# Kernel optimization log

Hardware: AMD Instinct MI355X
Metric: run time of the kernel (lower is better)

## Reference

```python
import jax, jax.numpy as jnp
import numpy as np

N_NODES = 50000
N_EDGES = 800000
IN, HID, OUT = 128, 128, 64


def _mean_agg(h, src, dst, n):
    # gather source-node features along edges, segment-mean into destination nodes
    msgs = h[src]                                          # [E, d]
    summ = jax.ops.segment_sum(msgs, dst, num_segments=n)  # [N, d]
    deg = jax.ops.segment_sum(jnp.ones((src.shape[0],), h.dtype), dst, num_segments=n)
    return summ / jnp.maximum(deg, 1.0)[:, None]           # zero-in-degree -> 0


def _sage_layer(h, src, dst, W_self, W_neigh, b, n):
    # DGL SAGEConv mean: fc_self(h) + fc_neigh(mean_neigh(h)) + bias
    agg = _mean_agg(h, src, dst, n)
    return h @ W_self + agg @ W_neigh + b


def setup_inputs() -> dict:
    key = jax.random.key(0)
    ks = jax.random.split(key, 8)
    s = 1.0 / np.sqrt(IN)
    return {
        "feat": jax.random.normal(ks[0], (N_NODES, IN), jnp.float32),
        "src": jax.random.randint(ks[1], (N_EDGES,), 0, N_NODES, jnp.int64),
        "dst": jax.random.randint(ks[2], (N_EDGES,), 0, N_NODES, jnp.int64),
        "W_self1": jax.random.normal(ks[3], (IN, HID), jnp.float32) * s,
        "W_neigh1": jax.random.normal(ks[4], (IN, HID), jnp.float32) * s,
        "b1": jnp.zeros((HID,), jnp.float32),
        "W_self2": jax.random.normal(ks[5], (HID, OUT), jnp.float32) * (1.0 / np.sqrt(HID)),
        "W_neigh2": jax.random.normal(ks[6], (HID, OUT), jnp.float32) * (1.0 / np.sqrt(HID)),
        "b2": jnp.zeros((OUT,), jnp.float32),
    }


def reference(feat, src, dst, W_self1, W_neigh1, b1, W_self2, W_neigh2, b2):
    n = feat.shape[0]
    h = _sage_layer(feat, src, dst, W_self1, W_neigh1, b1, n)
    h = jax.nn.relu(h)  # dropout is identity in eval mode
    h = _sage_layer(h, src, dst, W_self2, W_neigh2, b2, n)
    return h
```

## Files before the change

### kernel.cpp

```cpp
#include <hip/hip_runtime.h>

#define N_NODES 50000
#define N_EDGES 800000

typedef unsigned short ushort_t;
typedef unsigned int uint_t;
typedef __attribute__((ext_vector_type(8))) short bf16x8;
typedef __attribute__((ext_vector_type(4))) float f32x4;

#define NB 196
#define BCAP 6144
#define SDEPTH 16
#define EPB 1024
#define NBLK_BUCKET ((N_EDGES + EPB - 1) / EPB)

#define IOFF_ROWPTR  100000
#define IOFF_EIDX    150016
#define IOFF_BBASE   950016
#define IOFF_BCNT    950528
#define UOFF_WT      1920000
#define UOFF_FEATB   2000000
#define UOFF_AGG1B   8400000
#define UOFF_H1B     14800000
#define UOFF_P2B     21200000

__device__ __forceinline__ float bf2f(uint_t u) {
    return __uint_as_float(u << 16);
}
__device__ __forceinline__ uint_t f2bf(float f) {
    uint_t x = __float_as_uint(f);
    return (x + 0x7FFFu + ((x >> 16) & 1u)) >> 16;
}

__global__ __launch_bounds__(256) void bucket_kernel(const int* __restrict__ src,
                                                     const int* __restrict__ dst,
                                                     uint_t* __restrict__ bucket,
                                                     int* __restrict__ bcnt) {
    __shared__ uint_t stage[NB][SDEPTH];
    __shared__ int lcnt[NB];
    __shared__ int gbase[NB];
    int tid = threadIdx.x;
    for (int i = tid; i < NB; i += 256) lcnt[i] = 0;
    __syncthreads();
    int e0 = blockIdx.x * EPB;
#pragma unroll
    for (int it = 0; it < EPB / 256; ++it) {
        int e = e0 + it * 256 + tid;
        if (e < N_EDGES) {
            int d = dst[e], s = src[e];
            uint_t v = ((uint_t)d << 16) | (uint_t)s;
            int b = d >> 8;
            int slot = atomicAdd(&lcnt[b], 1);
            if (slot < SDEPTH) {
                stage[b][slot] = v;
            } else {
                int p = atomicAdd(&bcnt[b], 1);
                bucket[(long)b * BCAP + p] = v;
            }
        }
    }
    __syncthreads();
    if (tid < NB) {
        int n = min(lcnt[tid], SDEPTH);
        gbase[tid] = (n > 0) ? atomicAdd(&bcnt[tid], n) : 0;
    }
    __syncthreads();
    for (int s = tid; s < NB * SDEPTH; s += 256) {
        int b = s >> 4, i = s & (SDEPTH - 1);
        if (i < min(lcnt[b], SDEPTH))
            bucket[(long)b * BCAP + gbase[b] + i] = stage[b][i];
    }
}

__global__ __launch_bounds__(256) void scan196(const int* __restrict__ bcnt,
                                               int* __restrict__ bbase,
                                               int* __restrict__ rowptr) {
    __shared__ int sh[256];
    int tid = threadIdx.x;
    int v = (tid < NB) ? bcnt[tid] : 0;
    sh[tid] = v;
    __syncthreads();
    for (int off = 1; off < 256; off <<= 1) {
        int t = (tid >= off) ? sh[tid - off] : 0;
        __syncthreads();
        sh[tid] += t;
        __syncthreads();
    }
    if (tid < NB) bbase[tid] = sh[tid] - v;
    if (tid == NB - 1) rowptr[N_NODES] = sh[tid];
}

__global__ __launch_bounds__(512) void fill_bucket(const uint_t* __restrict__ bucket,
                                                   const int* __restrict__ bcnt,
                                                   const int* __restrict__ bbase,
                                                   int* __restrict__ rowptr,
                                                   int* __restrict__ eidx) {
    __shared__ int hist[256];
    __shared__ int excl[256];
    __shared__ int fp[256];
    int b = blockIdx.x, tid = threadIdx.x;
    if (tid < 256) { hist[tid] = 0; fp[tid] = 0; }
    __syncthreads();
    int n = bcnt[b];
    int base = bbase[b];
    int nodebase = b << 8;
    const uint_t* bk = bucket + (long)b * BCAP;
    for (int i = tid; i < n; i += 512) {
        int d = (int)(bk[i] >> 16) - nodebase;
        atomicAdd(&hist[d], 1);
    }
    __syncthreads();
    int v = 0;
    if (tid < 256) { v = hist[tid]; excl[tid] = v; }
    __syncthreads();
    for (int off = 1; off < 256; off <<= 1) {
        int t = 0;
        if (tid < 256 && tid >= off) t = excl[tid - off];
        __syncthreads();
        if (tid < 256) excl[tid] += t;
        __syncthreads();
    }
    if (tid < 256) {
        excl[tid] -= v;
        int node = nodebase + tid;
        if (node < N_NODES) rowptr[node] = base + excl[tid];
    }
    __syncthreads();
    for (int i = tid; i < n; i += 512) {
        uint_t vv = bk[i];
        int d = (int)(vv >> 16) - nodebase;
        int off = atomicAdd(&fp[d], 1);
        eidx[base + excl[d] + off] = (int)(vv & 0xFFFFu);
    }
}

__global__ __launch_bounds__(256) void cvt_kernel(const float* __restrict__ x,
                                                  ushort_t* __restrict__ y, int n4) {
    int i = blockIdx.x * 256 + threadIdx.x;
    if (i >= n4) return;
    float4 v = ((const float4*)x)[i];
    uint2 o;
    o.x = f2bf(v.x) | (f2bf(v.y) << 16);
    o.y = f2bf(v.z) | (f2bf(v.w) << 16);
    ((uint2*)y)[i] = o;
}

__global__ __launch_bounds__(256) void wprep_kernel(const float* __restrict__ Ws1,
                                                    const float* __restrict__ Wn1,
                                                    const float* __restrict__ Ws2,
                                                    const float* __restrict__ Wn2,
                                                    ushort_t* __restrict__ wT) {
    int i = blockIdx.x * 256 + threadIdx.x;
    if (i >= 49152) return;
    float v;
    if (i < 16384) {
        int n = i >> 7, k = i & 127;
        v = Ws1[k * 128 + n];
    } else if (i < 32768) {
        int j = i - 16384, n = j >> 7, k = j & 127;
        v = Wn1[k * 128 + n];
    } else if (i < 40960) {
        int j = i - 32768, n = j >> 7, k = j & 127;
        v = Wn2[k * 64 + n];
    } else {
        int j = i - 40960, n = j >> 7, k = j & 127;
        v = Ws2[k * 64 + n];
    }
    wT[i] = (ushort_t)f2bf(v);
}

__global__ __launch_bounds__(256) void gather128_kernel(const int* __restrict__ rowptr,
                                                        const int* __restrict__ eidx,
                                                        const ushort_t* __restrict__ xb,
                                                        ushort_t* __restrict__ aggb) {
    int node = blockIdx.x * 4 + (threadIdx.x >> 6);
    int lane = threadIdx.x & 63;
    if (node >= N_NODES) return;
    int q = lane >> 4;
    int sl = lane & 15;
    int beg = rowptr[node], end = rowptr[node + 1];
    float acc[8];
#pragma unroll
    for (int j = 0; j < 8; ++j) acc[j] = 0.f;

    int e = beg;
    for (; e + 7 < end; e += 8) {
        int sA = eidx[e + q];
        int sB = eidx[e + 4 + q];
        uint4 vA = *(const uint4*)(xb + (long)sA * 128 + sl * 8);
        uint4 vB = *(const uint4*)(xb + (long)sB * 128 + sl * 8);
        acc[0] += bf2f(vA.x & 0xffffu); acc[1] += bf2f(vA.x >> 16);
        acc[2] += bf2f(vA.y & 0xffffu); acc[3] += bf2f(vA.y >> 16);
        acc[4] += bf2f(vA.z & 0xffffu); acc[5] += bf2f(vA.z >> 16);
        acc[6] += bf2f(vA.w & 0xffffu); acc[7] += bf2f(vA.w >> 16);
        acc[0] += bf2f(vB.x & 0xffffu); acc[1] += bf2f(vB.x >> 16);
        acc[2] += bf2f(vB.y & 0xffffu); acc[3] += bf2f(vB.y >> 16);
        acc[4] += bf2f(vB.z & 0xffffu); acc[5] += bf2f(vB.z >> 16);
        acc[6] += bf2f(vB.w & 0xffffu); acc[7] += bf2f(vB.w >> 16);
    }
    for (; e + 3 < end; e += 4) {
        int s = eidx[e + q];
        uint4 v = *(const uint4*)(xb + (long)s * 128 + sl * 8);
        acc[0] += bf2f(v.x & 0xffffu); acc[1] += bf2f(v.x >> 16);
        acc[2] += bf2f(v.y & 0xffffu); acc[3] += bf2f(v.y >> 16);
        acc[4] += bf2f(v.z & 0xffffu); acc[5] += bf2f(v.z >> 16);
        acc[6] += bf2f(v.w & 0xffffu); acc[7] += bf2f(v.w >> 16);
    }
    if (e + q < end) {
        int s = eidx[e + q];
        uint4 v = *(const uint4*)(xb + (long)s * 128 + sl * 8);
        acc[0] += bf2f(v.x & 0xffffu); acc[1] += bf2f(v.x >> 16);
        acc[2] += bf2f(v.y & 0xffffu); acc[3] += bf2f(v.y >> 16);
        acc[4] += bf2f(v.z & 0xffffu); acc[5] += bf2f(v.z >> 16);
        acc[6] += bf2f(v.w & 0xffffu); acc[7] += bf2f(v.w >> 16);
    }
#pragma unroll
    for (int j = 0; j < 8; ++j) {
        acc[j] += __shfl_xor(acc[j], 16);
        acc[j] += __shfl_xor(acc[j], 32);
    }
    float inv = (end > beg) ? 1.0f / (float)(end - beg) : 0.f;
    if (lane < 16) {
        uint4 o;
        o.x = f2bf(acc[0] * inv) | (f2bf(acc[1] * inv) << 16);
        o.y = f2bf(acc[2] * inv) | (f2bf(acc[3] * inv) << 16);
        o.z = f2bf(acc[4] * inv) | (f2bf(acc[5] * inv) << 16);
        o.w = f2bf(acc[6] * inv) | (f2bf(acc[7] * inv) << 16);
        *(uint4*)(aggb + (long)node * 128 + sl * 8) = o;
    }
}

__global__ __launch_bounds__(256) void gather64_add_kernel(const int* __restrict__ rowptr,
                                                           const int* __restrict__ eidx,
                                                           const ushort_t* __restrict__ p2b,
                                                           float* __restrict__ out) {
    int node = blockIdx.x * 4 + (threadIdx.x >> 6);
    int lane = threadIdx.x & 63;
    if (node >= N_NODES) return;
    int q = lane >> 4;
    int sl = lane & 15;
    int beg = rowptr[node], end = rowptr[node + 1];
    float acc[4];
#pragma unroll
    for (int j = 0; j < 4; ++j) acc[j] = 0.f;

    int e = beg;
    for (; e + 7 < end; e += 8) {
        int sA = eidx[e + q];
        int sB = eidx[e + 4 + q];
        uint2 vA = *(const uint2*)(p2b + (long)sA * 64 + sl * 4);
        uint2 vB = *(const uint2*)(p2b + (long)sB * 64 + sl * 4);
        acc[0] += bf2f(vA.x & 0xffffu); acc[1] += bf2f(vA.x >> 16);
        acc[2] += bf2f(vA.y & 0xffffu); acc[3] += bf2f(vA.y >> 16);
        acc[0] += bf2f(vB.x & 0xffffu); acc[1] += bf2f(vB.x >> 16);
        acc[2] += bf2f(vB.y & 0xffffu); acc[3] += bf2f(vB.y >> 16);
    }
    for (; e + 3 < end; e += 4) {
        int s = eidx[e + q];
        uint2 v = *(const uint2*)(p2b + (long)s * 64 + sl * 4);
        acc[0] += bf2f(v.x & 0xffffu); acc[1] += bf2f(v.x >> 16);
        acc[2] += bf2f(v.y & 0xffffu); acc[3] += bf2f(v.y >> 16);
    }
    if (e + q < end) {
        int s = eidx[e + q];
        uint2 v = *(const uint2*)(p2b + (long)s * 64 + sl * 4);
        acc[0] += bf2f(v.x & 0xffffu); acc[1] += bf2f(v.x >> 16);
        acc[2] += bf2f(v.y & 0xffffu); acc[3] += bf2f(v.y >> 16);
    }
#pragma unroll
    for (int j = 0; j < 4; ++j) {
        acc[j] += __shfl_xor(acc[j], 16);
        acc[j] += __shfl_xor(acc[j], 32);
    }
    float inv = (end > beg) ? 1.0f / (float)(end - beg) : 0.f;
    if (lane < 16) {
        float4* po = (float4*)(out + (long)node * 64 + sl * 4);
        float4 o = *po;
        o.x += acc[0] * inv;
        o.y += acc[1] * inv;
        o.z += acc[2] * inv;
        o.w += acc[3] * inv;
        *po = o;
    }
}


__global__ __launch_bounds__(256) void gemm1_mfma(const ushort_t* __restrict__ featb,
                                                  const ushort_t* __restrict__ agg1b,
                                                  const ushort_t* __restrict__ wT,
                                                  const float* __restrict__ b,
                                                  ushort_t* __restrict__ h1b) {
    int lane = threadIdx.x & 63;
    int w = threadIdx.x >> 6;
    int mbase = blockIdx.x * 128 + w * 32;
    int lr = lane & 15;
    int kg = (lane >> 4) * 8;

    long r0 = mbase + lr;
    long r1 = mbase + 16 + lr;
    if (r0 > N_NODES - 1) r0 = N_NODES - 1;
    if (r1 > N_NODES - 1) r1 = N_NODES - 1;

    f32x4 acc[2][8];
#pragma unroll
    for (int mt = 0; mt < 2; ++mt)
#pragma unroll
        for (int nt = 0; nt < 8; ++nt) acc[mt][nt] = (f32x4){0.f, 0.f, 0.f, 0.f};

#pragma unroll
    for (int pass = 0; pass < 2; ++pass) {
        const ushort_t* a = pass ? agg1b : featb;
        const ushort_t* wt = wT + pass * (128 * 128);
#pragma unroll
        for (int ks = 0; ks < 4; ++ks) {
            int k = ks * 32 + kg;
            bf16x8 a0 = *(const bf16x8*)(a + r0 * 128 + k);
            bf16x8 a1 = *(const bf16x8*)(a + r1 * 128 + k);
#pragma unroll
            for (int nt = 0; nt < 8; ++nt) {
                bf16x8 bb = *(const bf16x8*)(wt + (nt * 16 + lr) * 128 + k);
                acc[0][nt] = __builtin_amdgcn_mfma_f32_16x16x32_bf16(a0, bb, acc[0][nt], 0, 0, 0);
                acc[1][nt] = __builtin_amdgcn_mfma_f32_16x16x32_bf16(a1, bb, acc[1][nt], 0, 0, 0);
            }
        }
    }

    int drow = (lane >> 4) * 4;
#pragma unroll
    for (int nt = 0; nt < 8; ++nt) {
        int n = nt * 16 + lr;
        float bias = b[n];
#pragma unroll
        for (int mt = 0; mt < 2; ++mt) {
#pragma unroll
            for (int r = 0; r < 4; ++r) {
                int row = mbase + mt * 16 + drow + r;
                if (row < N_NODES) {
                    float v = fmaxf(acc[mt][nt][r] + bias, 0.f);
                    h1b[(long)row * 128 + n] = (ushort_t)f2bf(v);
                }
            }
        }
    }
}

__global__ __launch_bounds__(256) void gemm2_mfma(const ushort_t* __restrict__ h1b,
                                                  const ushort_t* __restrict__ wT2,
                                                  const float* __restrict__ b2,
                                                  ushort_t* __restrict__ p2b,
                                                  float* __restrict__ out) {
    int lane = threadIdx.x & 63;
    int w = threadIdx.x >> 6;
    int mbase = blockIdx.x * 128 + w * 32;
    int lr = lane & 15;
    int kg = (lane >> 4) * 8;

    long r0 = mbase + lr;
    long r1 = mbase + 16 + lr;
    if (r0 > N_NODES - 1) r0 = N_NODES - 1;
    if (r1 > N_NODES - 1) r1 = N_NODES - 1;

    f32x4 accP[2][4], accO[2][4];
#pragma unroll
    for (int mt = 0; mt < 2; ++mt)
#pragma unroll
        for (int nt = 0; nt < 4; ++nt) {
            accP[mt][nt] = (f32x4){0.f, 0.f, 0.f, 0.f};
            accO[mt][nt] = (f32x4){0.f, 0.f, 0.f, 0.f};
        }

#pragma unroll
    for (int ks = 0; ks < 4; ++ks) {
        int k = ks * 32 + kg;
        bf16x8 a0 = *(const bf16x8*)(h1b + r0 * 128 + k);
        bf16x8 a1 = *(const bf16x8*)(h1b + r1 * 128 + k);
#pragma unroll
        for (int nt = 0; nt < 4; ++nt) {
            bf16x8 bn = *(const bf16x8*)(wT2 + (nt * 16 + lr) * 128 + k);
            bf16x8 bs = *(const bf16x8*)(wT2 + 8192 + (nt * 16 + lr) * 128 + k);
            accP[0][nt] = __builtin_amdgcn_mfma_f32_16x16x32_bf16(a0, bn, accP[0][nt], 0, 0, 0);
            accP[1][nt] = __builtin_amdgcn_mfma_f32_16x16x32_bf16(a1, bn, accP[1][nt], 0, 0, 0);
            accO[0][nt] = __builtin_amdgcn_mfma_f32_16x16x32_bf16(a0, bs, accO[0][nt], 0, 0, 0);
            accO[1][nt] = __builtin_amdgcn_mfma_f32_16x16x32_bf16(a1, bs, accO[1][nt], 0, 0, 0);
        }
    }

    int drow = (lane >> 4) * 4;
#pragma unroll
    for (int nt = 0; nt < 4; ++nt) {
        int n = nt * 16 + lr;
        float bias = b2[n];
#pragma unroll
        for (int mt = 0; mt < 2; ++mt) {
#pragma unroll
            for (int r = 0; r < 4; ++r) {
                int row = mbase + mt * 16 + drow + r;
                if (row < N_NODES) {
                    p2b[(long)row * 64 + n] = (ushort_t)f2bf(accP[mt][nt][r]);
                    out[(long)row * 64 + n] = accO[mt][nt][r] + bias;
                }
            }
        }
    }
}

extern "C" void kernel_launch(void* const* d_in, const int* in_sizes, int n_in,
                              void* d_out, int out_size, void* d_ws, size_t ws_size,
                              hipStream_t stream) {
    const float* feat = (const float*)d_in[0];
    const int* src    = (const int*)d_in[1];
    const int* dst    = (const int*)d_in[2];
    const float* Ws1  = (const float*)d_in[3];
    const float* Wn1  = (const float*)d_in[4];
    const float* b1   = (const float*)d_in[5];
    const float* Ws2  = (const float*)d_in[6];
    const float* Wn2  = (const float*)d_in[7];
    const float* b2   = (const float*)d_in[8];
    float* out = (float*)d_out;

    int* wsi      = (int*)d_ws;
    ushort_t* wsu = (ushort_t*)d_ws;
    int* rowptr   = wsi + IOFF_ROWPTR;
    int* eidx     = wsi + IOFF_EIDX;
    int* bbase    = wsi + IOFF_BBASE;
    int* bcnt     = wsi + IOFF_BCNT;
    ushort_t* wT    = wsu + UOFF_WT;
    ushort_t* featb = wsu + UOFF_FEATB;
    ushort_t* agg1b = wsu + UOFF_AGG1B;
    ushort_t* h1b   = wsu + UOFF_H1B;
    ushort_t* p2b   = wsu + UOFF_P2B;
    uint_t* bucket  = (uint_t*)(wsu + UOFF_H1B);

    hipMemsetAsync(bcnt, 0, NB * sizeof(int), stream);

    wprep_kernel<<<(49152 + 255) / 256, 256, 0, stream>>>(Ws1, Wn1, Ws2, Wn2, wT);
    cvt_kernel<<<(N_NODES * 128 / 4 + 255) / 256, 256, 0, stream>>>(feat, featb, N_NODES * 128 / 4);

    bucket_kernel<<<NBLK_BUCKET, 256, 0, stream>>>(src, dst, bucket, bcnt);
    scan196<<<1, 256, 0, stream>>>(bcnt, bbase, rowptr);
    fill_bucket<<<NB, 512, 0, stream>>>(bucket, bcnt, bbase, rowptr, eidx);

    gather128_kernel<<<(N_NODES + 3) / 4, 256, 0, stream>>>(rowptr, eidx, featb, agg1b);
    gemm1_mfma<<<(N_NODES + 127) / 128, 256, 0, stream>>>(featb, agg1b, wT, b1, h1b);

    gemm2_mfma<<<(N_NODES + 127) / 128, 256, 0, stream>>>(h1b, wT + 32768, b2, p2b, out);
    gather64_add_kernel<<<(N_NODES + 3) / 4, 256, 0, stream>>>(rowptr, eidx, p2b, out);
}
```

Before: 224.7 us.

## Merge prep kernels, widen fill_bucket blocks, unroll gathers to 16 edges

Fuses the feature bf16 conversion and the weight transpose into one prep kernel, saving a launch. Doubles the fill_bucket block size to 1024 threads so each bucket is processed with more parallelism. Unrolls both gather kernels to issue four independent row loads per iteration, raising memory-level parallelism. The cost is more register pressure and longer remainder handling for low-degree nodes.

```diff
diff --git a/kernel.cpp b/kernel.cpp
--- a/kernel.cpp
+++ b/kernel.cpp
@@ -13,6 +13,7 @@
 #define SDEPTH 16
 #define EPB 1024
 #define NBLK_BUCKET ((N_EDGES + EPB - 1) / EPB)
+#define NCVT4 (N_NODES * 128 / 4)
 
 #define IOFF_ROWPTR  100000
 #define IOFF_EIDX    150016
@@ -90,11 +91,11 @@
     if (tid == NB - 1) rowptr[N_NODES] = sh[tid];
 }
 
-__global__ __launch_bounds__(512) void fill_bucket(const uint_t* __restrict__ bucket,
-                                                   const int* __restrict__ bcnt,
-                                                   const int* __restrict__ bbase,
-                                                   int* __restrict__ rowptr,
-                                                   int* __restrict__ eidx) {
+__global__ __launch_bounds__(1024) void fill_bucket(const uint_t* __restrict__ bucket,
+                                                    const int* __restrict__ bcnt,
+                                                    const int* __restrict__ bbase,
+                                                    int* __restrict__ rowptr,
+                                                    int* __restrict__ eidx) {
     __shared__ int hist[256];
     __shared__ int excl[256];
     __shared__ int fp[256];
@@ -105,7 +106,7 @@
     int base = bbase[b];
     int nodebase = b << 8;
     const uint_t* bk = bucket + (long)b * BCAP;
-    for (int i = tid; i < n; i += 512) {
+    for (int i = tid; i < n; i += 1024) {
         int d = (int)(bk[i] >> 16) - nodebase;
         atomicAdd(&hist[d], 1);
     }
@@ -126,7 +127,7 @@
         if (node < N_NODES) rowptr[node] = base + excl[tid];
     }
     __syncthreads();
-    for (int i = tid; i < n; i += 512) {
+    for (int i = tid; i < n; i += 1024) {
         uint_t vv = bk[i];
         int d = (int)(vv >> 16) - nodebase;
         int off = atomicAdd(&fp[d], 1);
@@ -134,39 +135,39 @@
     }
 }
 
-__global__ __launch_bounds__(256) void cvt_kernel(const float* __restrict__ x,
-                                                  ushort_t* __restrict__ y, int n4) {
+__global__ __launch_bounds__(256) void prep_kernel(const float* __restrict__ feat,
+                                                   const float* __restrict__ Ws1,
+                                                   const float* __restrict__ Wn1,
+                                                   const float* __restrict__ Ws2,
+                                                   const float* __restrict__ Wn2,
+                                                   ushort_t* __restrict__ featb,
+                                                   ushort_t* __restrict__ wT) {
     int i = blockIdx.x * 256 + threadIdx.x;
-    if (i >= n4) return;
-    float4 v = ((const float4*)x)[i];
-    uint2 o;
-    o.x = f2bf(v.x) | (f2bf(v.y) << 16);
-    o.y = f2bf(v.z) | (f2bf(v.w) << 16);
-    ((uint2*)y)[i] = o;
-}
-
-__global__ __launch_bounds__(256) void wprep_kernel(const float* __restrict__ Ws1,
-                                                    const float* __restrict__ Wn1,
-                                                    const float* __restrict__ Ws2,
-                                                    const float* __restrict__ Wn2,
-                                                    ushort_t* __restrict__ wT) {
-    int i = blockIdx.x * 256 + threadIdx.x;
-    if (i >= 49152) return;
+    if (i < NCVT4) {
+        float4 v = ((const float4*)feat)[i];
+        uint2 o;
+        o.x = f2bf(v.x) | (f2bf(v.y) << 16);
+        o.y = f2bf(v.z) | (f2bf(v.w) << 16);
+        ((uint2*)featb)[i] = o;
+        return;
+    }
+    int j = i - NCVT4;
+    if (j >= 49152) return;
     float v;
-    if (i < 16384) {
-        int n = i >> 7, k = i & 127;
+    if (j < 16384) {
+        int n = j >> 7, k = j & 127;
         v = Ws1[k * 128 + n];
-    } else if (i < 32768) {
-        int j = i - 16384, n = j >> 7, k = j & 127;
+    } else if (j < 32768) {
+        int jj = j - 16384, n = jj >> 7, k = jj & 127;
         v = Wn1[k * 128 + n];
-    } else if (i < 40960) {
-        int j = i - 32768, n = j >> 7, k = j & 127;
+    } else if (j < 40960) {
+        int jj = j - 32768, n = jj >> 7, k = jj & 127;
         v = Wn2[k * 64 + n];
     } else {
-        int j = i - 40960, n = j >> 7, k = j & 127;
+        int jj = j - 40960, n = jj >> 7, k = jj & 127;
         v = Ws2[k * 64 + n];
     }
-    wT[i] = (ushort_t)f2bf(v);
+    wT[j] = (ushort_t)f2bf(v);
 }
 
 __global__ __launch_bounds__(256) void gather128_kernel(const int* __restrict__ rowptr,
@@ -184,19 +185,31 @@
     for (int j = 0; j < 8; ++j) acc[j] = 0.f;
 
     int e = beg;
-    for (; e + 7 < end; e += 8) {
-        int sA = eidx[e + q];
-        int sB = eidx[e + 4 + q];
-        uint4 vA = *(const uint4*)(xb + (long)sA * 128 + sl * 8);
-        uint4 vB = *(const uint4*)(xb + (long)sB * 128 + sl * 8);
-        acc[0] += bf2f(vA.x & 0xffffu); acc[1] += bf2f(vA.x >> 16);
-        acc[2] += bf2f(vA.y & 0xffffu); acc[3] += bf2f(vA.y >> 16);
-        acc[4] += bf2f(vA.z & 0xffffu); acc[5] += bf2f(vA.z >> 16);
-        acc[6] += bf2f(vA.w & 0xffffu); acc[7] += bf2f(vA.w >> 16);
-        acc[0] += bf2f(vB.x & 0xffffu); acc[1] += bf2f(vB.x >> 16);
-        acc[2] += bf2f(vB.y & 0xffffu); acc[3] += bf2f(vB.y >> 16);
-        acc[4] += bf2f(vB.z & 0xffffu); acc[5] += bf2f(vB.z >> 16);
-        acc[6] += bf2f(vB.w & 0xffffu); acc[7] += bf2f(vB.w >> 16);
+    for (; e + 15 < end; e += 16) {
+        int s0 = eidx[e + q];
+        int s1 = eidx[e + 4 + q];
+        int s2 = eidx[e + 8 + q];
+        int s3 = eidx[e + 12 + q];
+        uint4 v0 = *(const uint4*)(xb + (long)s0 * 128 + sl * 8);
+        uint4 v1 = *(const uint4*)(xb + (long)s1 * 128 + sl * 8);
+        uint4 v2 = *(const uint4*)(xb + (long)s2 * 128 + sl * 8);
+        uint4 v3 = *(const uint4*)(xb + (long)s3 * 128 + sl * 8);
+        acc[0] += bf2f(v0.x & 0xffffu); acc[1] += bf2f(v0.x >> 16);
+        acc[2] += bf2f(v0.y & 0xffffu); acc[3] += bf2f(v0.y >> 16);
+        acc[4] += bf2f(v0.z & 0xffffu); acc[5] += bf2f(v0.z >> 16);
+        acc[6] += bf2f(v0.w & 0xffffu); acc[7] += bf2f(v0.w >> 16);
+        acc[0] += bf2f(v1.x & 0xffffu); acc[1] += bf2f(v1.x >> 16);
+        acc[2] += bf2f(v1.y & 0xffffu); acc[3] += bf2f(v1.y >> 16);
+        acc[4] += bf2f(v1.z & 0xffffu); acc[5] += bf2f(v1.z >> 16);
+        acc[6] += bf2f(v1.w & 0xffffu); acc[7] += bf2f(v1.w >> 16);
+        acc[0] += bf2f(v2.x & 0xffffu); acc[1] += bf2f(v2.x >> 16);
+        acc[2] += bf2f(v2.y & 0xffffu); acc[3] += bf2f(v2.y >> 16);
+        acc[4] += bf2f(v2.z & 0xffffu); acc[5] += bf2f(v2.z >> 16);
+        acc[6] += bf2f(v2.w & 0xffffu); acc[7] += bf2f(v2.w >> 16);
+        acc[0] += bf2f(v3.x & 0xffffu); acc[1] += bf2f(v3.x >> 16);
+        acc[2] += bf2f(v3.y & 0xffffu); acc[3] += bf2f(v3.y >> 16);
+        acc[4] += bf2f(v3.z & 0xffffu); acc[5] += bf2f(v3.z >> 16);
+        acc[6] += bf2f(v3.w & 0xffffu); acc[7] += bf2f(v3.w >> 16);
     }
     for (; e + 3 < end; e += 4) {
         int s = eidx[e + q];
@@ -245,15 +258,23 @@
     for (int j = 0; j < 4; ++j) acc[j] = 0.f;
 
     int e = beg;
-    for (; e + 7 < end; e += 8) {
-        int sA = eidx[e + q];
-        int sB = eidx[e + 4 + q];
-        uint2 vA = *(const uint2*)(p2b + (long)sA * 64 + sl * 4);
-        uint2 vB = *(const uint2*)(p2b + (long)sB * 64 + sl * 4);
-        acc[0] += bf2f(vA.x & 0xffffu); acc[1] += bf2f(vA.x >> 16);
-        acc[2] += bf2f(vA.y & 0xffffu); acc[3] += bf2f(vA.y >> 16);
-        acc[0] += bf2f(vB.x & 0xffffu); acc[1] += bf2f(vB.x >> 16);
-        acc[2] += bf2f(vB.y & 0xffffu); acc[3] += bf2f(vB.y >> 16);
+    for (; e + 15 < end; e += 16) {
+        int s0 = eidx[e + q];
+        int s1 = eidx[e + 4 + q];
+        int s2 = eidx[e + 8 + q];
+        int s3 = eidx[e + 12 + q];
+        uint2 v0 = *(const uint2*)(p2b + (long)s0 * 64 + sl * 4);
+        uint2 v1 = *(const uint2*)(p2b + (long)s1 * 64 + sl * 4);
+        uint2 v2 = *(const uint2*)(p2b + (long)s2 * 64 + sl * 4);
+        uint2 v3 = *(const uint2*)(p2b + (long)s3 * 64 + sl * 4);
+        acc[0] += bf2f(v0.x & 0xffffu); acc[1] += bf2f(v0.x >> 16);
+        acc[2] += bf2f(v0.y & 0xffffu); acc[3] += bf2f(v0.y >> 16);
+        acc[0] += bf2f(v1.x & 0xffffu); acc[1] += bf2f(v1.x >> 16);
+        acc[2] += bf2f(v1.y & 0xffffu); acc[3] += bf2f(v1.y >> 16);
+        acc[0] += bf2f(v2.x & 0xffffu); acc[1] += bf2f(v2.x >> 16);
+        acc[2] += bf2f(v2.y & 0xffffu); acc[3] += bf2f(v2.y >> 16);
+        acc[0] += bf2f(v3.x & 0xffffu); acc[1] += bf2f(v3.x >> 16);
+        acc[2] += bf2f(v3.y & 0xffffu); acc[3] += bf2f(v3.y >> 16);
     }
     for (; e + 3 < end; e += 4) {
         int s = eidx[e + q];
@@ -433,12 +454,11 @@
 
     hipMemsetAsync(bcnt, 0, NB * sizeof(int), stream);
 
-    wprep_kernel<<<(49152 + 255) / 256, 256, 0, stream>>>(Ws1, Wn1, Ws2, Wn2, wT);
-    cvt_kernel<<<(N_NODES * 128 / 4 + 255) / 256, 256, 0, stream>>>(feat, featb, N_NODES * 128 / 4);
+    prep_kernel<<<(NCVT4 + 49152 + 255) / 256, 256, 0, stream>>>(feat, Ws1, Wn1, Ws2, Wn2, featb, wT);
 
     bucket_kernel<<<NBLK_BUCKET, 256, 0, stream>>>(src, dst, bucket, bcnt);
     scan196<<<1, 256, 0, stream>>>(bcnt, bbase, rowptr);
-    fill_bucket<<<NB, 512, 0, stream>>>(bucket, bcnt, bbase, rowptr, eidx);
+    fill_bucket<<<NB, 1024, 0, stream>>>(bucket, bcnt, bbase, rowptr, eidx);
 
     gather128_kernel<<<(N_NODES + 3) / 4, 256, 0, stream>>>(rowptr, eidx, featb, agg1b);
     gemm1_mfma<<<(N_NODES + 127) / 128, 256, 0, stream>>>(featb, agg1b, wT, b1, h1b);
```

Measured after the change: 220.7 us. Within noise of the previous version (-1.8%).
